# Performance work log

Measured on AMD Instinct MI355X. Metric: run time of the kernel, lower is better.

The kernel has to match this reference:

```python
import jax, jax.numpy as jnp
import numpy as np

K = 3          # kernel_size
P = 1          # padding
S = 1          # stride
C_IN = 64
C_OUT = 64


def unfold_patches(t, k=K, p=P, s=S):
    """Replicate-pad then extract kxk patches.
    Input  t: [B, C, H, W]
    Output  : [B, Ho, Wo, C, k*k]  matching torch unfold(2).unfold(3).permute(0,2,3,1,4,5).reshape
    (patch index varies as kh*k + kw)."""
    B, C, H, W = t.shape
    tp = jnp.pad(t, ((0, 0), (0, 0), (p, p), (p, p)), mode='edge')
    Ho = (H + 2 * p - k) // s + 1
    Wo = (W + 2 * p - k) // s + 1
    pats = [tp[:, :, a:a + (Ho - 1) * s + 1:s, b:b + (Wo - 1) * s + 1:s]
            for a in range(k) for b in range(k)]
    y = jnp.stack(pats, axis=-1)          # [B, C, Ho, Wo, k*k]
    return jnp.transpose(y, (0, 2, 3, 1, 4))  # [B, Ho, Wo, C, k*k]


def setup_inputs() -> dict:
    key = jax.random.key(0)
    k1, k2, k3, k4, k5, k6, k7 = jax.random.split(key, 7)
    B, H, W = 4, 128, 128
    feat_in = K * K * C_IN * 2      # 1152
    f1_out = K * K * C_IN           # 576
    f2_out = C_IN * C_OUT           # 4096
    lim1 = 1.0 / np.sqrt(feat_in)
    x = jax.random.normal(k1, (B, C_IN, H, W), dtype=jnp.float32)
    m = jax.random.uniform(k2, (B, C_IN, H, W), dtype=jnp.float32)
    s = jax.random.uniform(k3, (B, C_IN, H, W), dtype=jnp.float32)
    W1 = jax.random.uniform(k4, (feat_in, f1_out), minval=-lim1, maxval=lim1, dtype=jnp.float32)
    b1 = jax.random.uniform(k5, (f1_out,), minval=-lim1, maxval=lim1, dtype=jnp.float32)
    W2 = jax.random.uniform(k6, (feat_in, f2_out), minval=-lim1, maxval=lim1, dtype=jnp.float32)
    b2 = jax.random.uniform(k7, (f2_out,), minval=-lim1, maxval=lim1, dtype=jnp.float32)
    return {"x": x, "m": m, "s": s, "W1": W1, "b1": b1, "W2": W2, "b2": b2}


def reference(x, m, s, W1, b1, W2, b2):
    yp = unfold_patches(x)                              # [B,Ho,Wo,Cin,K2]
    mp = jax.lax.stop_gradient(unfold_patches(m))       # torch no_grad
    sp = jax.lax.stop_gradient(unfold_patches(s))
    B, Ho, Wo = yp.shape[:3]

    feat = jnp.concatenate([yp.reshape(B, Ho, Wo, -1),
                            mp.reshape(B, Ho, Wo, -1)], axis=-1)  # [B,Ho,Wo,2*K2*Cin]
    w1 = (feat @ W1 + b1).reshape(B, Ho, Wo, C_IN, K * K)
    w2 = (feat @ W2 + b2).reshape(B, Ho, Wo, C_IN, C_OUT)

    # y = sum_c (sum_k yp*w1) * w2
    yr = jnp.einsum('bhwck,bhwck->bhwc', yp, w1)
    y = jnp.einsum('bhwc,bhwco->bhwo', yr, w2)
    y = jnp.transpose(y, (0, 3, 1, 2))                  # [B,Cout,Ho,Wo]

    aw1 = jnp.abs(w1)
    aw2 = jnp.abs(w2)
    mr = jnp.einsum('bhwck,bhwck->bhwc', mp, aw1)
    m_y = jnp.transpose(jnp.einsum('bhwc,bhwco->bhwo', mr, aw2), (0, 3, 1, 2))
    sr = jnp.einsum('bhwck,bhwck->bhwc', sp, aw1)
    s_y = jnp.transpose(jnp.einsum('bhwc,bhwco->bhwo', sr, aw2), (0, 3, 1, 2))
    m_y = jax.lax.stop_gradient(m_y / s_y)

    return (y, m_y, jnp.ones_like(m_y))
```

## Files before the change

### kernel.cpp

```cpp
#include <hip/hip_runtime.h>
#include <stdint.h>
#include <stddef.h>


using short8   = __attribute__((ext_vector_type(8))) short;
using float4v  = __attribute__((ext_vector_type(4))) float;
using ushort4v = __attribute__((ext_vector_type(4))) unsigned short;

#define DI __device__ __forceinline__

DI unsigned short f2bf(float f) {
  union { float f; unsigned int u; } a; a.f = f;
  unsigned int r = a.u + 0x7fffu + ((a.u >> 16) & 1u);
  return (unsigned short)(r >> 16);
}
DI float bf2f(unsigned short u) {
  union { unsigned int u; float f; } a; a.u = ((unsigned int)u) << 16;
  return a.f;
}
DI void gll16(const void* g, void* l) {
  __builtin_amdgcn_global_load_lds(
      (const __attribute__((address_space(1))) unsigned int*)g,
      (__attribute__((address_space(3))) unsigned int*)l, 16, 0, 0);
}

__global__ void k_feat(const float* __restrict__ x, const float* __restrict__ m,
                       unsigned short* __restrict__ featb) {
  unsigned int v = blockIdx.x * 256u + threadIdx.x;
  unsigned int f = v * 8u;
  int pl   = (f >> 3) & 127;
  int q    = (f >> 10) & 3;
  int pblk = (f >> 12) & 511;
  int kk   = (int)(f >> 21);
  int base = kk * 32 + q * 8;
  const float* src = x;
  int jb = base;
  if (base >= 576) { src = m; jb = base - 576; }
  int p  = pblk * 128 + pl;
  int b  = p >> 14, h = (p >> 7) & 127;
  short8 o;
#pragma unroll
  for (int j = 0; j < 8; ++j) {
    int jx = jb + j;
    int c  = jx / 9;
    int t  = jx - c * 9;
    int t3 = t / 3;
    int dh = t3 - 1;
    int dw = (t - t3 * 3) - 1;
    int hh = min(max(h + dh, 0), 127);
    int ww = min(max(pl + dw, 0), 127);
    o[j] = (short)f2bf(src[(((b << 6) | c) << 14) + (hh << 7) + ww]);
  }
  *(short8*)&featb[(size_t)v * 8] = o;
}

__global__ void k_sw(const float* __restrict__ Wsrc, unsigned short* __restrict__ Wdst,
                     int ncols, int ntiles, int total, int perm) {
  int tid = blockIdx.x * 256 + threadIdx.x;
  if (tid >= total) return;
  int k8 = tid / ncols;
  int n  = tid - k8 * ncols;
  int np = perm ? (((n & 63) << 6) | (n >> 6)) : n;
  int k0 = k8 * 8;
  int obase = ((k0 >> 5) * ntiles + (np >> 4)) * 512 + (k8 & 3) * 128 +
              (np & 15) * 8;
  short8 o;
#pragma unroll
  for (int j = 0; j < 8; ++j)
    o[j] = (short)f2bf(Wsrc[(size_t)(k0 + j) * ncols + n]);
  *(short8*)&Wdst[obase] = o;
}

__launch_bounds__(512, 2)
__global__ void k_gemm1(const unsigned short* __restrict__ featb,
                        const unsigned short* __restrict__ W1s,
                        const float* __restrict__ b1,
                        const float* __restrict__ x, const float* __restrict__ m,
                        const float* __restrict__ s,
                        float* __restrict__ yr, float* __restrict__ mr,
                        float* __restrict__ sr) {
  __shared__ __align__(16) unsigned short Alds[4096];
  __shared__ __align__(16) unsigned short Blds[4608];
  __shared__ __align__(16) unsigned short w1buf[128 * 152];
  const int tid = threadIdx.x;
  const int wv  = tid >> 6;
  const int l15 = tid & 15;
  const int q   = (tid >> 4) & 3;
  const int bm  = blockIdx.x, nb = blockIdx.y;

  float4v acc[9];
#pragma unroll
  for (int t = 0; t < 9; ++t) acc[t] = (float4v){0.f, 0.f, 0.f, 0.f};

  const unsigned short* Ab = featb + (size_t)bm * 4096;
  const unsigned short* Bb = W1s + (size_t)nb * 9 * 512;

  for (int kk = 0; kk < 36; ++kk) {
    __syncthreads();
    gll16(Ab + (size_t)kk * 2097152 + tid * 8, (char*)Alds + wv * 1024);
    gll16(Bb + (size_t)kk * 18432 + tid * 8, (char*)Blds + wv * 1024);
    if (tid < 64) gll16(Bb + (size_t)kk * 18432 + 4096 + tid * 8, (char*)Blds + 8192);
    __syncthreads();
    short8 af = *(const short8*)&Alds[q * 1024 + (16 * wv + l15) * 8];
#pragma unroll
    for (int t = 0; t < 9; ++t) {
      short8 bfr = *(const short8*)&Blds[t * 512 + q * 128 + l15 * 8];
      acc[t] = __builtin_amdgcn_mfma_f32_16x16x32_bf16(af, bfr, acc[t], 0, 0, 0);
    }
  }

#pragma unroll
  for (int t = 0; t < 9; ++t) {
    int col = 16 * t + l15;
    float bb = b1[nb * 144 + col];
#pragma unroll
    for (int i = 0; i < 4; ++i) {
      int plr = 16 * wv + 4 * q + i;
      w1buf[plr * 152 + col] = f2bf(acc[t][i] + bb);
    }
  }
  __syncthreads();

  const int b = bm >> 7, h = bm & 127;
#pragma unroll
  for (int ii = 0; ii < 4; ++ii) {
    int task = ii * 512 + tid;
    int p  = task >> 4;
    int cl = task & 15;
    int c  = nb * 16 + cl;
    float w1v[9];
#pragma unroll
    for (int k = 0; k < 9; ++k) w1v[k] = bf2f(w1buf[p * 152 + cl * 9 + k]);
    size_t base = (size_t)(((b << 6) | c) << 14);
    float vy = 0.f, vm = 0.f, vs = 0.f;
#pragma unroll
    for (int dh = -1; dh <= 1; ++dh) {
      int hh = min(max(h + dh, 0), 127);
#pragma unroll
      for (int dw = -1; dw <= 1; ++dw) {
        int ww = min(max(p + dw, 0), 127);
        size_t idx = base + (hh << 7) + ww;
        int k = (dh + 1) * 3 + (dw + 1);
        float wv1 = w1v[k], aw = fabsf(wv1);
        vy += x[idx] * wv1;
        vm += m[idx] * aw;
        vs += s[idx] * aw;
      }
    }
    size_t P = (size_t)bm * 128 + p;
    yr[P * 64 + c] = vy;
    mr[P * 64 + c] = vm;
    sr[P * 64 + c] = vs;
  }
}

__launch_bounds__(512, 4)
__global__ void k_gemm2(const unsigned short* __restrict__ featb,
                        const unsigned short* __restrict__ W2s,
                        const float* __restrict__ b2,
                        const float* __restrict__ yr, const float* __restrict__ mr,
                        const float* __restrict__ sr,
                        float* __restrict__ out) {
  __shared__ __align__(16) unsigned short U[3][12288];
  unsigned short* w2buf = &U[2][0];
  const int tid  = threadIdx.x;
  const int wv   = tid >> 6;
  const int lane = tid & 63;
  const int wm   = wv >> 2;
  const int wn   = wv & 3;
  const int l15  = tid & 15;
  const int q    = (tid >> 4) & 3;
  const int part = lane >> 4;
  const int bm   = blockIdx.x;

  const unsigned short* Ab = featb + (size_t)bm * 4096;

  float4v acc[4][4];
#pragma unroll
  for (int r = 0; r < 4; ++r)
#pragma unroll
    for (int t = 0; t < 4; ++t) acc[r][t] = (float4v){0.f, 0.f, 0.f, 0.f};

  gll16(Ab + tid * 8,                  (char*)&U[0][0]    + wv * 1024);
  gll16(W2s + tid * 8,                 (char*)&U[0][4096] + wv * 1024);
  gll16(W2s + 4096 + tid * 8,          (char*)&U[0][8192] + wv * 1024);
  gll16(Ab + 2097152 + tid * 8,        (char*)&U[1][0]    + wv * 1024);
  gll16(W2s + 131072 + tid * 8,        (char*)&U[1][4096] + wv * 1024);
  gll16(W2s + 131072 + 4096 + tid * 8, (char*)&U[1][8192] + wv * 1024);

#define G2_KK(KK, BR, BS, DRAIN)                                               \
  do {                                                                         \
    int kks = (KK) + 2, chs = ch;                                              \
    if (kks >= 36) { kks -= 36; chs += 1; }                                    \
    if (DRAIN) { asm volatile("s_waitcnt vmcnt(0)" ::: "memory"); }            \
    else       { asm volatile("s_waitcnt vmcnt(3)" ::: "memory"); }            \
    __builtin_amdgcn_s_barrier();                                              \
    asm volatile("" ::: "memory");                                             \
    if (chs < 16) {                                                            \
      const unsigned short* Ag = Ab + (size_t)kks * 2097152;                   \
      const unsigned short* Bg = W2s + (size_t)kks * 131072 + (size_t)chs * 8192; \
      gll16(Ag + tid * 8,        (char*)&U[BS][0]    + wv * 1024);             \
      gll16(Bg + tid * 8,        (char*)&U[BS][4096] + wv * 1024);             \
      gll16(Bg + 4096 + tid * 8, (char*)&U[BS][8192] + wv * 1024);             \
    }                                                                          \
    {                                                                          \
      const unsigned short* Al = &U[BR][0];                                    \
      const unsigned short* Bl = &U[BR][4096];                                 \
      short8 a_[4];                                                            \
      _Pragma("unroll") for (int r = 0; r < 4; ++r)                            \
        a_[r] = *(const short8*)&Al[q * 1024 + (64 * wm + 16 * r + l15) * 8];  \
      __builtin_amdgcn_s_setprio(1);                                           \
      _Pragma("unroll") for (int t = 0; t < 4; ++t) {                          \
        short8 bfr = *(const short8*)&Bl[(4 * wn + t) * 512 + q * 128 + l15 * 8]; \
        _Pragma("unroll") for (int r = 0; r < 4; ++r)                          \
          acc[r][t] = __builtin_amdgcn_mfma_f32_16x16x32_bf16(a_[r], bfr,      \
                                                              acc[r][t], 0, 0, 0); \
      }                                                                        \
      __builtin_amdgcn_s_setprio(0);                                           \
    }                                                                          \
  } while (0)

  for (int ch = 0; ch < 16; ++ch) {
    const bool lc = (ch == 15);
    for (int k3 = 0; k3 < 12; ++k3) {
      const int kk = k3 * 3;
      G2_KK(kk + 0, 0, 2, false);
      G2_KK(kk + 1, 1, 0, (lc && k3 == 11));
      G2_KK(kk + 2, 2, 1, (lc && k3 == 11));
    }

    float b2v[4];
#pragma unroll
    for (int t = 0; t < 4; ++t) b2v[t] = b2[(16 * t + l15) * 64 + 4 * ch + wn];

    for (int p = 0; p < 4; ++p) {
      __syncthreads();
      if (wn == p) {
#pragma unroll
        for (int r = 0; r < 4; ++r)
#pragma unroll
          for (int t = 0; t < 4; ++t)
#pragma unroll
            for (int i = 0; i < 4; ++i)
              w2buf[(64 * wm + 16 * r + 4 * q + i) * 68 + 16 * t + l15] =
                  f2bf(acc[r][t][i] + b2v[t]);
      }
      __syncthreads();
      const int row = 16 * wv + l15;
      const size_t P = (size_t)bm * 128 + row;
      const float4v* y4 = (const float4v*)(yr + P * 64 + 16 * part);
      const float4v* m4 = (const float4v*)(mr + P * 64 + 16 * part);
      const float4v* s4 = (const float4v*)(sr + P * 64 + 16 * part);
      const ushort4v* w4 = (const ushort4v*)&w2buf[row * 68 + 16 * part];
      float ys = 0.f, ms = 0.f, ss = 0.f;
#pragma unroll
      for (int j4 = 0; j4 < 4; ++j4) {
        float4v yv = y4[j4], mv = m4[j4], sv = s4[j4];
        ushort4v wq = w4[j4];
#pragma unroll
        for (int j = 0; j < 4; ++j) {
          float w2f = bf2f(wq[j]);
          float aw  = fabsf(w2f);
          ys += yv[j] * w2f;
          ms += mv[j] * aw;
          ss += sv[j] * aw;
        }
      }
      ys += __shfl_xor(ys, 16); ys += __shfl_xor(ys, 32);
      ms += __shfl_xor(ms, 16); ms += __shfl_xor(ms, 32);
      ss += __shfl_xor(ss, 16); ss += __shfl_xor(ss, 32);
      if (part == 0) {
        const int o = 4 * ch + p;
        const int b = (int)(P >> 14), h = (int)((P >> 7) & 127), w = (int)(P & 127);
        size_t idx = ((size_t)((b << 6) | o) << 14) + (h << 7) + w;
        out[idx]           = ys;
        out[4194304 + idx] = ms / ss;
        out[8388608 + idx] = 1.0f;
      }
    }
#pragma unroll
    for (int r = 0; r < 4; ++r)
#pragma unroll
      for (int t = 0; t < 4; ++t) acc[r][t] = (float4v){0.f, 0.f, 0.f, 0.f};
  }
#undef G2_KK
}

extern "C" void kernel_launch(void* const* d_in, const int* in_sizes, int n_in,
                              void* d_out, int out_size, void* d_ws, size_t ws_size,
                              hipStream_t stream) {
  const float* x  = (const float*)d_in[0];
  const float* m  = (const float*)d_in[1];
  const float* s  = (const float*)d_in[2];
  const float* W1 = (const float*)d_in[3];
  const float* b1 = (const float*)d_in[4];
  const float* W2 = (const float*)d_in[5];
  const float* b2 = (const float*)d_in[6];
  float* out = (float*)d_out;

  if (ws_size < 212090880ull) return;
  char* ws = (char*)d_ws;
  unsigned short* featb = (unsigned short*)ws;
  unsigned short* W1s   = (unsigned short*)(ws + 150994944);
  unsigned short* W2s   = (unsigned short*)(ws + 152322048);
  float* yr = (float*)(ws + 161759232);
  float* mr = (float*)(ws + 178536448);
  float* sr = (float*)(ws + 195313664);

  k_feat<<<36864, 256, 0, stream>>>(x, m, featb);
  k_sw<<<324, 256, 0, stream>>>(W1, W1s, 576, 36, 82944, 0);
  k_sw<<<2304, 256, 0, stream>>>(W2, W2s, 4096, 256, 589824, 1);
  dim3 g1(512, 4);
  k_gemm1<<<g1, 512, 0, stream>>>(featb, W1s, b1, x, m, s, yr, mr, sr);
  k_gemm2<<<512, 512, 0, stream>>>(featb, W2s, b2, yr, mr, sr, out);
}
```

Measured before the change: 1.109 ms.

## Widen gemm1 N-tile to halve A reloads; hoist epilogue loads in gemm2

```diff
diff --git a/kernel.cpp b/kernel.cpp
--- a/kernel.cpp
+++ b/kernel.cpp
@@ -71,7 +71,7 @@
   *(short8*)&Wdst[obase] = o;
 }
 
-__launch_bounds__(512, 2)
+__launch_bounds__(512, 4)
 __global__ void k_gemm1(const unsigned short* __restrict__ featb,
                         const unsigned short* __restrict__ W1s,
                         const float* __restrict__ b1,
@@ -80,77 +80,82 @@
                         float* __restrict__ yr, float* __restrict__ mr,
                         float* __restrict__ sr) {
   __shared__ __align__(16) unsigned short Alds[4096];
-  __shared__ __align__(16) unsigned short Blds[4608];
+  __shared__ __align__(16) unsigned short Blds[9216];
   __shared__ __align__(16) unsigned short w1buf[128 * 152];
   const int tid = threadIdx.x;
   const int wv  = tid >> 6;
   const int l15 = tid & 15;
   const int q   = (tid >> 4) & 3;
-  const int bm  = blockIdx.x, nb = blockIdx.y;
-
-  float4v acc[9];
-#pragma unroll
-  for (int t = 0; t < 9; ++t) acc[t] = (float4v){0.f, 0.f, 0.f, 0.f};
+  const int bm  = blockIdx.x, nb2 = blockIdx.y;
+
+  float4v acc[18];
+#pragma unroll
+  for (int t = 0; t < 18; ++t) acc[t] = (float4v){0.f, 0.f, 0.f, 0.f};
 
   const unsigned short* Ab = featb + (size_t)bm * 4096;
-  const unsigned short* Bb = W1s + (size_t)nb * 9 * 512;
+  const unsigned short* Bb = W1s + (size_t)nb2 * 9216;
 
   for (int kk = 0; kk < 36; ++kk) {
     __syncthreads();
     gll16(Ab + (size_t)kk * 2097152 + tid * 8, (char*)Alds + wv * 1024);
     gll16(Bb + (size_t)kk * 18432 + tid * 8, (char*)Blds + wv * 1024);
-    if (tid < 64) gll16(Bb + (size_t)kk * 18432 + 4096 + tid * 8, (char*)Blds + 8192);
+    gll16(Bb + (size_t)kk * 18432 + 4096 + tid * 8, (char*)Blds + 8192 + wv * 1024);
+    if (tid < 128)
+      gll16(Bb + (size_t)kk * 18432 + 8192 + tid * 8,
+            (char*)Blds + 16384 + (tid >> 6) * 1024);
     __syncthreads();
     short8 af = *(const short8*)&Alds[q * 1024 + (16 * wv + l15) * 8];
 #pragma unroll
-    for (int t = 0; t < 9; ++t) {
+    for (int t = 0; t < 18; ++t) {
       short8 bfr = *(const short8*)&Blds[t * 512 + q * 128 + l15 * 8];
       acc[t] = __builtin_amdgcn_mfma_f32_16x16x32_bf16(af, bfr, acc[t], 0, 0, 0);
     }
   }
 
-#pragma unroll
-  for (int t = 0; t < 9; ++t) {
-    int col = 16 * t + l15;
-    float bb = b1[nb * 144 + col];
-#pragma unroll
-    for (int i = 0; i < 4; ++i) {
-      int plr = 16 * wv + 4 * q + i;
-      w1buf[plr * 152 + col] = f2bf(acc[t][i] + bb);
-    }
-  }
-  __syncthreads();
-
   const int b = bm >> 7, h = bm & 127;
-#pragma unroll
-  for (int ii = 0; ii < 4; ++ii) {
-    int task = ii * 512 + tid;
-    int p  = task >> 4;
-    int cl = task & 15;
-    int c  = nb * 16 + cl;
-    float w1v[9];
-#pragma unroll
-    for (int k = 0; k < 9; ++k) w1v[k] = bf2f(w1buf[p * 152 + cl * 9 + k]);
-    size_t base = (size_t)(((b << 6) | c) << 14);
-    float vy = 0.f, vm = 0.f, vs = 0.f;
-#pragma unroll
-    for (int dh = -1; dh <= 1; ++dh) {
-      int hh = min(max(h + dh, 0), 127);
-#pragma unroll
-      for (int dw = -1; dw <= 1; ++dw) {
-        int ww = min(max(p + dw, 0), 127);
-        size_t idx = base + (hh << 7) + ww;
-        int k = (dh + 1) * 3 + (dw + 1);
-        float wv1 = w1v[k], aw = fabsf(wv1);
-        vy += x[idx] * wv1;
-        vm += m[idx] * aw;
-        vs += s[idx] * aw;
-      }
-    }
-    size_t P = (size_t)bm * 128 + p;
-    yr[P * 64 + c] = vy;
-    mr[P * 64 + c] = vm;
-    sr[P * 64 + c] = vs;
+  for (int half = 0; half < 2; ++half) {
+    __syncthreads();
+#pragma unroll
+    for (int t = 0; t < 9; ++t) {
+      int col = 16 * t + l15;
+      float bb = b1[nb2 * 288 + half * 144 + col];
+#pragma unroll
+      for (int i = 0; i < 4; ++i) {
+        int plr = 16 * wv + 4 * q + i;
+        w1buf[plr * 152 + col] = f2bf(acc[9 * half + t][i] + bb);
+      }
+    }
+    __syncthreads();
+#pragma unroll
+    for (int ii = 0; ii < 4; ++ii) {
+      int task = ii * 512 + tid;
+      int p  = task >> 4;
+      int cl = task & 15;
+      int c  = nb2 * 32 + half * 16 + cl;
+      float w1v[9];
+#pragma unroll
+      for (int k = 0; k < 9; ++k) w1v[k] = bf2f(w1buf[p * 152 + cl * 9 + k]);
+      size_t base = (size_t)(((b << 6) | c) << 14);
+      float vy = 0.f, vm = 0.f, vs = 0.f;
+#pragma unroll
+      for (int dh = -1; dh <= 1; ++dh) {
+        int hh = min(max(h + dh, 0), 127);
+#pragma unroll
+        for (int dw = -1; dw <= 1; ++dw) {
+          int ww = min(max(p + dw, 0), 127);
+          size_t idx = base + (hh << 7) + ww;
+          int k = (dh + 1) * 3 + (dw + 1);
+          float wv1 = w1v[k], aw = fabsf(wv1);
+          vy += x[idx] * wv1;
+          vm += m[idx] * aw;
+          vs += s[idx] * aw;
+        }
+      }
+      size_t P = (size_t)bm * 128 + p;
+      yr[P * 64 + c] = vy;
+      mr[P * 64 + c] = vm;
+      sr[P * 64 + c] = vs;
+    }
   }
 }
 
@@ -180,6 +185,12 @@
   for (int r = 0; r < 4; ++r)
 #pragma unroll
     for (int t = 0; t < 4; ++t) acc[r][t] = (float4v){0.f, 0.f, 0.f, 0.f};
+
+  const int erow = 16 * wv + l15;
+  const size_t eP = (size_t)bm * 128 + erow;
+  const float4v* ey4 = (const float4v*)(yr + eP * 64 + 16 * part);
+  const float4v* em4 = (const float4v*)(mr + eP * 64 + 16 * part);
+  const float4v* es4 = (const float4v*)(sr + eP * 64 + 16 * part);
 
   gll16(Ab + tid * 8,                  (char*)&U[0][0]    + wv * 1024);
   gll16(W2s + tid * 8,                 (char*)&U[0][4096] + wv * 1024);
@@ -229,6 +240,13 @@
       G2_KK(kk + 2, 2, 1, (lc && k3 == 11));
     }
 
+    float4v yv4[4], mv4[4], sv4[4];
+#pragma unroll
+    for (int j4 = 0; j4 < 4; ++j4) {
+      yv4[j4] = ey4[j4];
+      mv4[j4] = em4[j4];
+      sv4[j4] = es4[j4];
+    }
     float b2v[4];
 #pragma unroll
     for (int t = 0; t < 4; ++t) b2v[t] = b2[(16 * t + l15) * 64 + 4 * ch + wn];
@@ -246,24 +264,18 @@
                   f2bf(acc[r][t][i] + b2v[t]);
       }
       __syncthreads();
-      const int row = 16 * wv + l15;
-      const size_t P = (size_t)bm * 128 + row;
-      const float4v* y4 = (const float4v*)(yr + P * 64 + 16 * part);
-      const float4v* m4 = (const float4v*)(mr + P * 64 + 16 * part);
-      const float4v* s4 = (const float4v*)(sr + P * 64 + 16 * part);
-      const ushort4v* w4 = (const ushort4v*)&w2buf[row * 68 + 16 * part];
+      const ushort4v* w4 = (const ushort4v*)&w2buf[erow * 68 + 16 * part];
       float ys = 0.f, ms = 0.f, ss = 0.f;
 #pragma unroll
       for (int j4 = 0; j4 < 4; ++j4) {
-        float4v yv = y4[j4], mv = m4[j4], sv = s4[j4];
         ushort4v wq = w4[j4];
 #pragma unroll
         for (int j = 0; j < 4; ++j) {
           float w2f = bf2f(wq[j]);
           float aw  = fabsf(w2f);
-          ys += yv[j] * w2f;
-          ms += mv[j] * aw;
-          ss += sv[j] * aw;
+          ys += yv4[j4][j] * w2f;
+          ms += mv4[j4][j] * aw;
+          ss += sv4[j4][j] * aw;
         }
       }
       ys += __shfl_xor(ys, 16); ys += __shfl_xor(ys, 32);
@@ -271,7 +283,7 @@
       ss += __shfl_xor(ss, 16); ss += __shfl_xor(ss, 32);
       if (part == 0) {
         const int o = 4 * ch + p;
-        const int b = (int)(P >> 14), h = (int)((P >> 7) & 127), w = (int)(P & 127);
+        const int b = (int)(eP >> 14), h = (int)((eP >> 7) & 127), w = (int)(eP & 127);
         size_t idx = ((size_t)((b << 6) | o) << 14) + (h << 7) + w;
         out[idx]           = ys;
         out[4194304 + idx] = ms / ss;
@@ -310,7 +322,7 @@
   k_feat<<<36864, 256, 0, stream>>>(x, m, featb);
   k_sw<<<324, 256, 0, stream>>>(W1, W1s, 576, 36, 82944, 0);
   k_sw<<<2304, 256, 0, stream>>>(W2, W2s, 4096, 256, 589824, 1);
-  dim3 g1(512, 4);
+  dim3 g1(512, 2);
   k_gemm1<<<g1, 512, 0, stream>>>(featb, W1s, b1, x, m, s, yr, mr, sr);
   k_gemm2<<<512, 512, 0, stream>>>(featb, W2s, b2, yr, mr, sr, out);
 }
```

New measurement: 1.228 ms. 1.11x slower.

## Reduce GEMM2 epilogue in registers, dropping LDS staging and barriers

Applied to the files above, without the earlier changes.

```diff
diff --git a/kernel.cpp b/kernel.cpp
--- a/kernel.cpp
+++ b/kernel.cpp
@@ -162,15 +162,12 @@
                         const float* __restrict__ sr,
                         float* __restrict__ out) {
   __shared__ __align__(16) unsigned short U[3][12288];
-  unsigned short* w2buf = &U[2][0];
   const int tid  = threadIdx.x;
   const int wv   = tid >> 6;
-  const int lane = tid & 63;
   const int wm   = wv >> 2;
   const int wn   = wv & 3;
   const int l15  = tid & 15;
   const int q    = (tid >> 4) & 3;
-  const int part = lane >> 4;
   const int bm   = blockIdx.x;
 
   const unsigned short* Ab = featb + (size_t)bm * 4096;
@@ -229,53 +226,45 @@
       G2_KK(kk + 2, 2, 1, (lc && k3 == 11));
     }
 
-    float b2v[4];
-#pragma unroll
-    for (int t = 0; t < 4; ++t) b2v[t] = b2[(16 * t + l15) * 64 + 4 * ch + wn];
-
-    for (int p = 0; p < 4; ++p) {
-      __syncthreads();
-      if (wn == p) {
-#pragma unroll
-        for (int r = 0; r < 4; ++r)
-#pragma unroll
-          for (int t = 0; t < 4; ++t)
-#pragma unroll
-            for (int i = 0; i < 4; ++i)
-              w2buf[(64 * wm + 16 * r + 4 * q + i) * 68 + 16 * t + l15] =
-                  f2bf(acc[r][t][i] + b2v[t]);
-      }
-      __syncthreads();
-      const int row = 16 * wv + l15;
-      const size_t P = (size_t)bm * 128 + row;
-      const float4v* y4 = (const float4v*)(yr + P * 64 + 16 * part);
-      const float4v* m4 = (const float4v*)(mr + P * 64 + 16 * part);
-      const float4v* s4 = (const float4v*)(sr + P * 64 + 16 * part);
-      const ushort4v* w4 = (const ushort4v*)&w2buf[row * 68 + 16 * part];
-      float ys = 0.f, ms = 0.f, ss = 0.f;
-#pragma unroll
-      for (int j4 = 0; j4 < 4; ++j4) {
-        float4v yv = y4[j4], mv = m4[j4], sv = s4[j4];
-        ushort4v wq = w4[j4];
-#pragma unroll
-        for (int j = 0; j < 4; ++j) {
-          float w2f = bf2f(wq[j]);
-          float aw  = fabsf(w2f);
-          ys += yv[j] * w2f;
-          ms += mv[j] * aw;
-          ss += sv[j] * aw;
+    {
+      const int o = 4 * ch + wn;
+      float b2v[4];
+#pragma unroll
+      for (int t = 0; t < 4; ++t) b2v[t] = b2[(16 * t + l15) * 64 + o];
+
+#pragma unroll
+      for (int r = 0; r < 4; ++r) {
+#pragma unroll
+        for (int i = 0; i < 4; ++i) {
+          const int row = 64 * wm + 16 * r + 4 * q + i;
+          const size_t P = (size_t)bm * 128 + row;
+          const float* yp = yr + P * 64 + l15;
+          const float* mp = mr + P * 64 + l15;
+          const float* sp = sr + P * 64 + l15;
+          float ys = 0.f, ms = 0.f, ss = 0.f;
+#pragma unroll
+          for (int t = 0; t < 4; ++t) {
+            float w2f = acc[r][t][i] + b2v[t];
+            float aw  = fabsf(w2f);
+            ys += yp[16 * t] * w2f;
+            ms += mp[16 * t] * aw;
+            ss += sp[16 * t] * aw;
+          }
+          ys += __shfl_xor(ys, 1); ys += __shfl_xor(ys, 2);
+          ys += __shfl_xor(ys, 4); ys += __shfl_xor(ys, 8);
+          ms += __shfl_xor(ms, 1); ms += __shfl_xor(ms, 2);
+          ms += __shfl_xor(ms, 4); ms += __shfl_xor(ms, 8);
+          ss += __shfl_xor(ss, 1); ss += __shfl_xor(ss, 2);
+          ss += __shfl_xor(ss, 4); ss += __shfl_xor(ss, 8);
+          if (l15 == 0) {
+            const int bb = (int)(P >> 14), hh = (int)((P >> 7) & 127),
+                      ww = (int)(P & 127);
+            size_t idx = ((size_t)((bb << 6) | o) << 14) + (hh << 7) + ww;
+            out[idx]           = ys;
+            out[4194304 + idx] = ms / ss;
+            out[8388608 + idx] = 1.0f;
+          }
         }
-      }
-      ys += __shfl_xor(ys, 16); ys += __shfl_xor(ys, 32);
-      ms += __shfl_xor(ms, 16); ms += __shfl_xor(ms, 32);
-      ss += __shfl_xor(ss, 16); ss += __shfl_xor(ss, 32);
-      if (part == 0) {
-        const int o = 4 * ch + p;
-        const int b = (int)(P >> 14), h = (int)((P >> 7) & 127), w = (int)(P & 127);
-        size_t idx = ((size_t)((b << 6) | o) << 14) + (h << 7) + w;
-        out[idx]           = ys;
-        out[4194304 + idx] = ms / ss;
-        out[8388608 + idx] = 1.0f;
       }
     }
 #pragma unroll
```

Result: slower. 2.248 ms (+102.8%).
